# Optimization experiments

Measured on AMD Instinct MI355X. Metric: run time of the kernel, lower is better.

The kernel has to match this reference:

```python
import jax, jax.numpy as jnp
import numpy as np

N, M, D_IN, D_TXT, D_OUT, H = 4096, 1024, 512, 512, 512, 8
DH = D_OUT // H


def positional_encoding(n, dim):
    # Matches PositionalEncoding: freq = exp((arange(dim//2)/dim)*ln(10000)),
    # x = pos/freq -> [L, dim//2], interleave (sin, cos) pairs -> [L, dim].
    pos = jnp.arange(n, dtype=jnp.float32)
    freq = jnp.exp((jnp.arange(dim // 2, dtype=jnp.float32) / dim) * jnp.log(jnp.float32(10000.0)))
    x = pos[:, None] / freq  # [L, dim//2]
    pe = jnp.stack((jnp.sin(x), jnp.cos(x)), axis=-1)  # [L, dim//2, 2]
    return pe.reshape(n, dim)


def setup_inputs() -> dict:
    key = jax.random.key(0)
    k1, k2, k3, k4, k5, k6 = jax.random.split(key, 6)
    s = 0.02
    return {
        "video_features": jax.random.normal(k1, (N, D_IN), dtype=jnp.float32),
        "text_features": jax.random.normal(k2, (M, D_TXT), dtype=jnp.float32),
        "Wq": jax.random.normal(k3, (H, D_IN, DH), dtype=jnp.float32) * s,
        "Wk": jax.random.normal(k4, (H, D_TXT, DH), dtype=jnp.float32) * s,
        "Wv": jax.random.normal(k5, (H, D_TXT, DH), dtype=jnp.float32) * s,
        "Wout": jax.random.normal(k6, (D_OUT, D_IN), dtype=jnp.float32) * s,
    }


def reference(video_features, text_features, Wq, Wk, Wv, Wout):
    # Batched over heads instead of the original per-head Python loop (same math).
    Q = jnp.einsum('nd,hde->hne', video_features, Wq)   # [H, N, DH]
    K = jnp.einsum('md,hde->hme', text_features, Wk)    # [H, M, DH]
    V = jnp.einsum('md,hde->hme', text_features, Wv)    # [H, M, DH]
    energies = jnp.einsum('hne,hme->hnm', Q, K)         # no scaling in original
    att = jax.nn.softmax(energies, axis=-1)             # dropout omitted (eval mode)
    y = jnp.einsum('hnm,hme->hne', att, V)              # [H, N, DH]
    y = jnp.transpose(y, (1, 0, 2)).reshape(video_features.shape[0], -1)  # concat heads
    y = y @ Wout                                        # [N, D_IN]
    y = y + positional_encoding(y.shape[0], y.shape[1])
    return y
```

## Files before the change

### kernel.cpp

```cpp
#include <hip/hip_runtime.h>
#include <hip/hip_bf16.h>
#include <math.h>

#define N_TOK 4096
#define M_TOK 1024
#define DMODEL 512
#define NHEAD 8
#define DHEAD 64
#define LOG2E 1.44269504f

typedef __attribute__((ext_vector_type(8))) short short8;
typedef __attribute__((ext_vector_type(4))) float f32x4;
typedef __attribute__((ext_vector_type(4))) float float4v;

static __device__ __forceinline__ short f2bf(float f) {
    union { float f; unsigned u; } v; v.f = f;
    unsigned r = v.u + 0x7fffu + ((v.u >> 16) & 1u);
    return (short)(r >> 16);
}

__global__ __launch_bounds__(256) void pack_kernel(
        const float* __restrict__ xv, const float* __restrict__ xt,
        const float* __restrict__ wq, const float* __restrict__ wk,
        const float* __restrict__ wv, const float* __restrict__ wo,
        short* __restrict__ xvb, short* __restrict__ xtb,
        short* __restrict__ wqb, short* __restrict__ wkb,
        short* __restrict__ wvb, short* __restrict__ wob) {
    int bid = blockIdx.x;
    int t = threadIdx.x;
    if (bid < 256) {
        __shared__ float lds[64][65];
        const float* src;
        short* dst;
        int srstride;
        int dr0, dc0;
        if (bid < 192) {
            int mat = bid >> 6;
            int hb = bid & 63;
            int h = hb >> 3, dt = hb & 7;
            const float* W = (mat == 0) ? wq : (mat == 1) ? wk : wv;
            src = W + (size_t)h * (DMODEL * DHEAD) + (size_t)(dt * 64) * DHEAD;
            srstride = DHEAD;
            dst = (mat == 0) ? wqb : (mat == 1) ? wkb : wvb;
            dr0 = h * 64;
            dc0 = dt * 64;
        } else {
            int b = bid - 192;
            int rt = b >> 3, ct = b & 7;
            src = wo + (size_t)(rt * 64) * DMODEL + ct * 64;
            srstride = DMODEL;
            dst = wob;
            dr0 = ct * 64;
            dc0 = rt * 64;
        }
        {
            int r = t >> 2, c0 = (t & 3) * 16;
            const float* s = src + (size_t)r * srstride + c0;
            #pragma unroll
            for (int j = 0; j < 4; j++) {
                float4v v = *(const float4v*)(s + j * 4);
                lds[r][c0 + j * 4 + 0] = v[0];
                lds[r][c0 + j * 4 + 1] = v[1];
                lds[r][c0 + j * 4 + 2] = v[2];
                lds[r][c0 + j * 4 + 3] = v[3];
            }
        }
        __syncthreads();
        {
            int outr = t >> 2, c0 = (t & 3) * 16;
            short8 o0, o1;
            #pragma unroll
            for (int j = 0; j < 8; j++) {
                o0[j] = f2bf(lds[c0 + j][outr]);
                o1[j] = f2bf(lds[c0 + 8 + j][outr]);
            }
            short* d = dst + (size_t)(dr0 + outr) * DMODEL + dc0 + c0;
            *(short8*)d = o0;
            *(short8*)(d + 8) = o1;
        }
        return;
    }
    int idx = (bid - 256) * 256 + t;
    int stride = (gridDim.x - 256) * 256;
    const int CXV = N_TOK * DMODEL / 8;
    const int CXT = M_TOK * DMODEL / 8;
    for (int c = idx; c < CXV; c += stride) {
        float4v f0 = *(const float4v*)&xv[c * 8];
        float4v f1 = *(const float4v*)&xv[c * 8 + 4];
        short8 o;
        #pragma unroll
        for (int j = 0; j < 4; j++) { o[j] = f2bf(f0[j]); o[j + 4] = f2bf(f1[j]); }
        *(short8*)&xvb[c * 8] = o;
    }
    for (int c = idx; c < CXT; c += stride) {
        float4v f0 = *(const float4v*)&xt[c * 8];
        float4v f1 = *(const float4v*)&xt[c * 8 + 4];
        short8 o;
        #pragma unroll
        for (int j = 0; j < 4; j++) { o[j] = f2bf(f0[j]); o[j + 4] = f2bf(f1[j]); }
        *(short8*)&xtb[c * 8] = o;
    }
}

template<typename EPI>
static __device__ __forceinline__ void gemm_body8(const short* __restrict__ A,
                                                  const short* __restrict__ BT,
                                                  int m0, int n0, EPI epi) {
    __shared__ __align__(16) short As[64][72];
    __shared__ __align__(16) short Bs[64][72];
    int t = threadIdx.x;
    int lane = t & 63, w = t >> 6;
    int wr = w & 3, wc = w >> 2;
    int l15 = lane & 15, g = lane >> 4;

    int row = t >> 3, c0 = (t & 7) * 8;
    const short* gA = A + (size_t)(m0 + row) * DMODEL + c0;
    const short* gB = BT + (size_t)(n0 + row) * DMODEL + c0;

    short8 ra = *(const short8*)gA;
    short8 rb = *(const short8*)gB;

    f32x4 acc[2] = {};
    #pragma unroll
    for (int step = 0; step < DMODEL / 64; ++step) {
        *(short8*)&As[row][c0] = ra;
        *(short8*)&Bs[row][c0] = rb;
        __syncthreads();
        if (step < DMODEL / 64 - 1) {
            gA += 64; gB += 64;
            ra = *(const short8*)gA;
            rb = *(const short8*)gB;
        }
        #pragma unroll
        for (int ks = 0; ks < 2; ks++) {
            short8 a = *(short8*)&As[wr * 16 + l15][ks * 32 + g * 8];
            #pragma unroll
            for (int fc = 0; fc < 2; fc++) {
                short8 b = *(short8*)&Bs[wc * 32 + fc * 16 + l15][ks * 32 + g * 8];
                acc[fc] = __builtin_amdgcn_mfma_f32_16x16x32_bf16(a, b, acc[fc], 0, 0, 0);
            }
        }
        __syncthreads();
    }
    #pragma unroll
    for (int fc = 0; fc < 2; fc++)
        #pragma unroll
        for (int r = 0; r < 4; r++) {
            int orow = m0 + wr * 16 + g * 4 + r;
            int ocol = n0 + wc * 32 + fc * 16 + l15;
            epi(orow, ocol, acc[fc][r]);
        }
}

__global__ __launch_bounds__(512) void gemmKV(const short* __restrict__ xtb,
                                              const short* __restrict__ wkb,
                                              const short* __restrict__ wvb,
                                              short* __restrict__ kbm,
                                              short* __restrict__ vbt) {
    int bx = blockIdx.x;
    if (bx < 128) {
        gemm_body8(xtb, wkb, (bx >> 3) * 64, (bx & 7) * 64,
                   [&](int row, int col, float v) { kbm[(size_t)row * DMODEL + col] = f2bf(v * LOG2E); });
    } else {
        int b = bx - 128;
        gemm_body8(xtb, wvb, (b >> 3) * 64, (b & 7) * 64,
                   [&](int row, int col, float v) { vbt[(size_t)col * M_TOK + row] = f2bf(v); });
    }
}

__global__ __launch_bounds__(512) void gemmOut(const short* __restrict__ A,
                                               const short* __restrict__ BT,
                                               float* __restrict__ Cout) {
    __shared__ float ifreq[256];
    if (threadIdx.x < 256)
        ifreq[threadIdx.x] = __expf(-(float)threadIdx.x * (9.210340371976184f / 512.0f));
    __syncthreads();
    gemm_body8(A, BT, blockIdx.x * 64, blockIdx.y * 64,
               [&](int row, int col, float v) {
                   float x = (float)row * ifreq[col >> 1];
                   float s, c;
                   __sincosf(x, &s, &c);
                   Cout[(size_t)row * DMODEL + col] = v + ((col & 1) ? c : s);
               });
}

struct AttnS {
    short Ks[2][64][72];
    short Vt[2][64][72];
    short Ps[8][16][72];
};
struct MergeS {
    f32x4 macc[4][4][64];
    f32x4 mrs[4][64];
};
struct GemmS {
    short As[64][72];
    short Bs[64][72];
};
union AttnU { AttnS a; MergeS m; GemmS g; };

__global__ __launch_bounds__(512) void attn_kernel(const short* __restrict__ xvb,
                                                   const short* __restrict__ wqb,
                                                   const short* __restrict__ Kb,
                                                   const short* __restrict__ VbT,
                                                   short* __restrict__ Yb) {
    __shared__ __align__(16) AttnU u;
    __shared__ __align__(16) short Qs[64][72];

    int bid = blockIdx.x;
    int h = bid & 7;
    int n0 = (bid >> 3) * 64;
    int t = threadIdx.x;
    int lane = t & 63, w = t >> 6;
    int qg = w & 3, kh = w >> 2;
    int l15 = lane & 15, g = lane >> 4;

    {
        int row = t >> 3, c0 = (t & 7) * 8;
        const short* gA = xvb + (size_t)(n0 + row) * DMODEL + c0;
        const short* gB = wqb + (size_t)(h * DHEAD + row) * DMODEL + c0;
        short8 ra = *(const short8*)gA;
        short8 rb = *(const short8*)gB;
        int wr = w & 3, wc = w >> 2;
        f32x4 qacc[2] = {};
        #pragma unroll
        for (int step = 0; step < DMODEL / 64; ++step) {
            *(short8*)&u.g.As[row][c0] = ra;
            *(short8*)&u.g.Bs[row][c0] = rb;
            __syncthreads();
            if (step < DMODEL / 64 - 1) {
                gA += 64; gB += 64;
                ra = *(const short8*)gA;
                rb = *(const short8*)gB;
            }
            #pragma unroll
            for (int ks = 0; ks < 2; ks++) {
                short8 a = *(short8*)&u.g.As[wr * 16 + l15][ks * 32 + g * 8];
                #pragma unroll
                for (int fc = 0; fc < 2; fc++) {
                    short8 b = *(short8*)&u.g.Bs[wc * 32 + fc * 16 + l15][ks * 32 + g * 8];
                    qacc[fc] = __builtin_amdgcn_mfma_f32_16x16x32_bf16(a, b, qacc[fc], 0, 0, 0);
                }
            }
            __syncthreads();
        }
        #pragma unroll
        for (int fc = 0; fc < 2; fc++)
            #pragma unroll
            for (int r = 0; r < 4; r++)
                Qs[wr * 16 + g * 4 + r][wc * 32 + fc * 16 + l15] = f2bf(qacc[fc][r]);
        __syncthreads();
    }

    short8 qa0 = *(short8*)&Qs[qg * 16 + l15][g * 8];
    short8 qa1 = *(short8*)&Qs[qg * 16 + l15][32 + g * 8];

    int sh = t >> 8;
    int tt = t & 255;
    int row = tt >> 2, c0 = (tt & 3) * 16;
    const short* gK = Kb + (size_t)(sh * 512 + row) * DMODEL + h * DHEAD + c0;
    const short* gV = VbT + (size_t)(h * DHEAD + row) * M_TOK + sh * 512 + c0;

    short8 k0 = *(const short8*)gK;
    short8 k1 = *(const short8*)(gK + 8);
    short8 v0 = *(const short8*)gV;
    short8 v1 = *(const short8*)(gV + 8);

    f32x4 acc[4] = {};
    f32x4 rsum = {};

    for (int it = 0; it < 8; ++it) {
        *(short8*)&u.a.Ks[sh][row][c0]     = k0;
        *(short8*)&u.a.Ks[sh][row][c0 + 8] = k1;
        *(short8*)&u.a.Vt[sh][row][c0]     = v0;
        *(short8*)&u.a.Vt[sh][row][c0 + 8] = v1;
        __syncthreads();
        if (it < 7) {
            gK += (size_t)64 * DMODEL;
            gV += 64;
            k0 = *(const short8*)gK;
            k1 = *(const short8*)(gK + 8);
            v0 = *(const short8*)gV;
            v1 = *(const short8*)(gV + 8);
        }
        #pragma unroll
        for (int kt = 0; kt < 4; kt++) {
            short8 kf0 = *(short8*)&u.a.Ks[kh][kt * 16 + l15][g * 8];
            short8 kf1 = *(short8*)&u.a.Ks[kh][kt * 16 + l15][32 + g * 8];
            f32x4 e = {};
            e = __builtin_amdgcn_mfma_f32_16x16x32_bf16(qa0, kf0, e, 0, 0, 0);
            e = __builtin_amdgcn_mfma_f32_16x16x32_bf16(qa1, kf1, e, 0, 0, 0);
            #pragma unroll
            for (int r = 0; r < 4; r++) {
                float p = exp2f(e[r]);
                rsum[r] += p;
                u.a.Ps[w][g * 4 + r][kt * 16 + l15] = f2bf(p);
            }
        }
        #pragma unroll
        for (int kb2 = 0; kb2 < 2; kb2++) {
            short8 pa = *(short8*)&u.a.Ps[w][l15][kb2 * 32 + g * 8];
            #pragma unroll
            for (int nt = 0; nt < 4; nt++) {
                short8 vf = *(short8*)&u.a.Vt[kh][nt * 16 + l15][kb2 * 32 + g * 8];
                acc[nt] = __builtin_amdgcn_mfma_f32_16x16x32_bf16(pa, vf, acc[nt], 0, 0, 0);
            }
        }
        __syncthreads();
    }

    if (kh == 1) {
        #pragma unroll
        for (int nt = 0; nt < 4; nt++) u.m.macc[qg][nt][lane] = acc[nt];
        u.m.mrs[qg][lane] = rsum;
    }
    __syncthreads();
    if (kh == 0) {
        #pragma unroll
        for (int nt = 0; nt < 4; nt++) acc[nt] += u.m.macc[qg][nt][lane];
        rsum += u.m.mrs[qg][lane];
        #pragma unroll
        for (int r = 0; r < 4; r++) {
            float s = rsum[r];
            s += __shfl_xor(s, 1);
            s += __shfl_xor(s, 2);
            s += __shfl_xor(s, 4);
            s += __shfl_xor(s, 8);
            rsum[r] = s;
        }
        #pragma unroll
        for (int nt = 0; nt < 4; nt++)
            #pragma unroll
            for (int r = 0; r < 4; r++) {
                float y = acc[nt][r] / rsum[r];
                Yb[(size_t)(n0 + qg * 16 + g * 4 + r) * DMODEL + h * DHEAD + nt * 16 + l15] = f2bf(y);
            }
    }
}

extern "C" void kernel_launch(void* const* d_in, const int* in_sizes, int n_in,
                              void* d_out, int out_size, void* d_ws, size_t ws_size,
                              hipStream_t stream) {
    const float* xv = (const float*)d_in[0];
    const float* xt = (const float*)d_in[1];
    const float* wq = (const float*)d_in[2];
    const float* wk = (const float*)d_in[3];
    const float* wv = (const float*)d_in[4];
    const float* wo = (const float*)d_in[5];

    short* xvb = (short*)d_ws;
    short* xtb = xvb + N_TOK * DMODEL;
    short* wqb = xtb + M_TOK * DMODEL;
    short* wkb = wqb + DMODEL * DMODEL;
    short* wvb = wkb + DMODEL * DMODEL;
    short* wob = wvb + DMODEL * DMODEL;
    short* kbm = wob + DMODEL * DMODEL;
    short* vbt = kbm + M_TOK * DMODEL;
    short* yb  = vbt + M_TOK * DMODEL;

    pack_kernel<<<1280, 256, 0, stream>>>(xv, xt, wq, wk, wv, wo,
                                          xvb, xtb, wqb, wkb, wvb, wob);
    gemmKV<<<256, 512, 0, stream>>>(xtb, wkb, wvb, kbm, vbt);
    attn_kernel<<<512, 512, 0, stream>>>(xvb, wqb, kbm, vbt, yb);
    gemmOut<<<dim3(64, 8), 512, 0, stream>>>(yb, wob, (float*)d_out);
}
```

Before: 50.98 us.

## Remap attention warps to 32-query tiles with key-split and four-way merge

Warps in the attention kernel now each own 32 query rows and split the keys of each 64-key tile into halves, where before each warp had 16 query rows and all 64 keys. Each K and V fragment loaded from shared memory now feeds two query subtiles, which raises MFMA work per LDS read. The P scratch tile is reshaped to 32x40 to match. Partial outputs and row sums are now merged across four warps through shared memory instead of two, which adds more merge traffic and register use.

```diff
diff --git a/kernel.cpp b/kernel.cpp
--- a/kernel.cpp
+++ b/kernel.cpp
@@ -187,11 +187,11 @@
 struct AttnS {
     short Ks[2][64][72];
     short Vt[2][64][72];
-    short Ps[8][16][72];
+    short Ps[8][32][40];
 };
 struct MergeS {
-    f32x4 macc[4][4][64];
-    f32x4 mrs[4][64];
+    f32x4 macc[2][3][2][4][64];
+    f32x4 mrs[2][3][2][64];
 };
 struct GemmS {
     short As[64][72];
@@ -212,7 +212,7 @@
     int n0 = (bid >> 3) * 64;
     int t = threadIdx.x;
     int lane = t & 63, w = t >> 6;
-    int qg = w & 3, kh = w >> 2;
+    int qg = w >> 2, kh = (w >> 1) & 1, half = w & 1;
     int l15 = lane & 15, g = lane >> 4;
 
     {
@@ -252,8 +252,12 @@
         __syncthreads();
     }
 
-    short8 qa0 = *(short8*)&Qs[qg * 16 + l15][g * 8];
-    short8 qa1 = *(short8*)&Qs[qg * 16 + l15][32 + g * 8];
+    short8 qa[2][2];
+    #pragma unroll
+    for (int s = 0; s < 2; s++)
+        #pragma unroll
+        for (int d = 0; d < 2; d++)
+            qa[s][d] = *(short8*)&Qs[qg * 32 + s * 16 + l15][d * 32 + g * 8];
 
     int sh = t >> 8;
     int tt = t & 255;
@@ -266,8 +270,8 @@
     short8 v0 = *(const short8*)gV;
     short8 v1 = *(const short8*)(gV + 8);
 
-    f32x4 acc[4] = {};
-    f32x4 rsum = {};
+    f32x4 acc[2][4] = {};
+    f32x4 rsum[2] = {};
 
     for (int it = 0; it < 8; ++it) {
         *(short8*)&u.a.Ks[sh][row][c0]     = k0;
@@ -284,57 +288,75 @@
             v1 = *(const short8*)(gV + 8);
         }
         #pragma unroll
-        for (int kt = 0; kt < 4; kt++) {
+        for (int ktl = 0; ktl < 2; ktl++) {
+            int kt = half * 2 + ktl;
             short8 kf0 = *(short8*)&u.a.Ks[kh][kt * 16 + l15][g * 8];
             short8 kf1 = *(short8*)&u.a.Ks[kh][kt * 16 + l15][32 + g * 8];
-            f32x4 e = {};
-            e = __builtin_amdgcn_mfma_f32_16x16x32_bf16(qa0, kf0, e, 0, 0, 0);
-            e = __builtin_amdgcn_mfma_f32_16x16x32_bf16(qa1, kf1, e, 0, 0, 0);
+            #pragma unroll
+            for (int s = 0; s < 2; s++) {
+                f32x4 e = {};
+                e = __builtin_amdgcn_mfma_f32_16x16x32_bf16(qa[s][0], kf0, e, 0, 0, 0);
+                e = __builtin_amdgcn_mfma_f32_16x16x32_bf16(qa[s][1], kf1, e, 0, 0, 0);
+                #pragma unroll
+                for (int r = 0; r < 4; r++) {
+                    float p = exp2f(e[r]);
+                    rsum[s][r] += p;
+                    u.a.Ps[w][s * 16 + g * 4 + r][ktl * 16 + l15] = f2bf(p);
+                }
+            }
+        }
+        short8 pa[2];
+        #pragma unroll
+        for (int s = 0; s < 2; s++) pa[s] = *(short8*)&u.a.Ps[w][s * 16 + l15][g * 8];
+        #pragma unroll
+        for (int nt = 0; nt < 4; nt++) {
+            short8 vf = *(short8*)&u.a.Vt[kh][nt * 16 + l15][half * 32 + g * 8];
+            #pragma unroll
+            for (int s = 0; s < 2; s++)
+                acc[s][nt] = __builtin_amdgcn_mfma_f32_16x16x32_bf16(pa[s], vf, acc[s][nt], 0, 0, 0);
+        }
+        __syncthreads();
+    }
+
+    int grp = w & 3;
+    if (grp != 0) {
+        #pragma unroll
+        for (int s = 0; s < 2; s++) {
+            #pragma unroll
+            for (int nt = 0; nt < 4; nt++) u.m.macc[qg][grp - 1][s][nt][lane] = acc[s][nt];
+            u.m.mrs[qg][grp - 1][s][lane] = rsum[s];
+        }
+    }
+    __syncthreads();
+    if (grp == 0) {
+        #pragma unroll
+        for (int gi = 0; gi < 3; gi++)
+            #pragma unroll
+            for (int s = 0; s < 2; s++) {
+                #pragma unroll
+                for (int nt = 0; nt < 4; nt++) acc[s][nt] += u.m.macc[qg][gi][s][nt][lane];
+                rsum[s] += u.m.mrs[qg][gi][s][lane];
+            }
+        #pragma unroll
+        for (int s = 0; s < 2; s++)
             #pragma unroll
             for (int r = 0; r < 4; r++) {
-                float p = exp2f(e[r]);
-                rsum[r] += p;
-                u.a.Ps[w][g * 4 + r][kt * 16 + l15] = f2bf(p);
-            }
-        }
-        #pragma unroll
-        for (int kb2 = 0; kb2 < 2; kb2++) {
-            short8 pa = *(short8*)&u.a.Ps[w][l15][kb2 * 32 + g * 8];
-            #pragma unroll
-            for (int nt = 0; nt < 4; nt++) {
-                short8 vf = *(short8*)&u.a.Vt[kh][nt * 16 + l15][kb2 * 32 + g * 8];
-                acc[nt] = __builtin_amdgcn_mfma_f32_16x16x32_bf16(pa, vf, acc[nt], 0, 0, 0);
-            }
-        }
-        __syncthreads();
-    }
-
-    if (kh == 1) {
-        #pragma unroll
-        for (int nt = 0; nt < 4; nt++) u.m.macc[qg][nt][lane] = acc[nt];
-        u.m.mrs[qg][lane] = rsum;
-    }
-    __syncthreads();
-    if (kh == 0) {
-        #pragma unroll
-        for (int nt = 0; nt < 4; nt++) acc[nt] += u.m.macc[qg][nt][lane];
-        rsum += u.m.mrs[qg][lane];
-        #pragma unroll
-        for (int r = 0; r < 4; r++) {
-            float s = rsum[r];
-            s += __shfl_xor(s, 1);
-            s += __shfl_xor(s, 2);
-            s += __shfl_xor(s, 4);
-            s += __shfl_xor(s, 8);
-            rsum[r] = s;
-        }
-        #pragma unroll
-        for (int nt = 0; nt < 4; nt++)
-            #pragma unroll
-            for (int r = 0; r < 4; r++) {
-                float y = acc[nt][r] / rsum[r];
-                Yb[(size_t)(n0 + qg * 16 + g * 4 + r) * DMODEL + h * DHEAD + nt * 16 + l15] = f2bf(y);
-            }
+                float v = rsum[s][r];
+                v += __shfl_xor(v, 1);
+                v += __shfl_xor(v, 2);
+                v += __shfl_xor(v, 4);
+                v += __shfl_xor(v, 8);
+                rsum[s][r] = v;
+            }
+        #pragma unroll
+        for (int s = 0; s < 2; s++)
+            #pragma unroll
+            for (int nt = 0; nt < 4; nt++)
+                #pragma unroll
+                for (int r = 0; r < 4; r++) {
+                    float y = acc[s][nt][r] / rsum[s][r];
+                    Yb[(size_t)(n0 + qg * 32 + s * 16 + g * 4 + r) * DMODEL + h * DHEAD + nt * 16 + l15] = f2bf(y);
+                }
     }
 }
 
```

Result: slower. 60.22 us (+18.1%).
